# Kernel optimization log

Measured on AMD Instinct MI355X. Metric: run time of the kernel, lower is better.

## Reference

```python
import jax, jax.numpy as jnp
import numpy as np

SPU_ZERO = float(np.sqrt(0.5))  # sqrt(|spu(0)|), spu(0) = -0.5


def spu(x):
    # spu(x) = x^2 - 0.5 for x >= 0, sigmoid(-x) - 1 for x < 0
    return jnp.where(x >= 0, x * x - 0.5, jax.nn.sigmoid(-x) - 1.0)


def dspu(x):
    s = jax.nn.sigmoid(-x)
    return jnp.where(x >= 0, 2.0 * x, -s * (1.0 - s))


def setup_inputs() -> dict:
    key = jax.random.key(0)
    k1, k2, k3 = jax.random.split(key, 3)
    N = 16777216
    lower = jax.random.normal(k1, (N,), dtype=jnp.float32)
    width = jnp.abs(jax.random.normal(k2, (N,), dtype=jnp.float32)) + 1e-3
    upper = lower + width
    t = jax.random.uniform(k3, (N,), dtype=jnp.float32)
    x = lower + t * width  # concrete point inside the interval
    return {"x": x, "lower_bounds": lower, "upper_bounds": upper}


def reference(x, lower_bounds, upper_bounds):
    l = lower_bounds
    u = upper_bounds
    sl = spu(l)
    su = spu(u)
    slope = (su - sl) / (u - l)  # chord slope
    chord_b = sl - slope * l

    # case 2 (l >= 0) tangent at midpoint
    a2 = (u + l) * 0.5
    wl2 = dspu(a2)
    bl2 = spu(a2) - a2 * wl2

    # case 3 (l < 0 <= u, u >= spu_zero) tangent at max(mid, spu_zero)
    a3 = jnp.maximum(a2, SPU_ZERO)
    wl3 = dspu(a3)
    bl3 = spu(a3) - a3 * wl3

    # case 4 (l < 0, 0 < u < spu_zero)
    flat4 = sl > su
    wu4 = jnp.where(flat4, 0.0, slope)
    bu4 = jnp.where(flat4, jnp.maximum(sl, su), chord_b)

    c1 = u <= 0
    c2 = l >= 0
    c3 = u >= SPU_ZERO

    w_u = jnp.where(c1, 0.0,
          jnp.where(c2, u + l,
          jnp.where(c3, slope, wu4)))
    b_u = jnp.where(c1, sl,
          jnp.where(c2, -u * l + 0.5,  # -u*l - spu(0)
          jnp.where(c3, chord_b, bu4)))
    w_l = jnp.where(c1, slope,
          jnp.where(c2, wl2,
          jnp.where(c3, wl3, 0.0)))
    b_l = jnp.where(c1, chord_b,
          jnp.where(c2, bl2,
          jnp.where(c3, bl3, -0.5)))  # spu(0) = -0.5

    out = spu(x)
    # weights are eye with modified diagonal -> diagonal matmul is elementwise
    new_lower = w_l * l + b_l
    new_upper = w_u * u + b_u
    return (out, new_lower, new_upper)
```

## Files before the change

### kernel.cpp

```cpp
#include <hip/hip_runtime.h>
#include <math.h>

#define SPU_ZERO 0.70710678118654752440f

__device__ __forceinline__ float spu_f(float x) {
    if (x >= 0.0f) return x * x - 0.5f;
    float s = 1.0f / (1.0f + expf(x));
    return s - 1.0f;
}

__device__ __forceinline__ float dspu_f(float x) {
    if (x >= 0.0f) return 2.0f * x;
    float s = 1.0f / (1.0f + expf(x));
    return -s * (1.0f - s);
}

__device__ __forceinline__ void spu_transform(float x, float l, float u,
                                              float& o, float& nl, float& nu) {
    float sl = spu_f(l);
    float su = spu_f(u);
    float slope = (su - sl) / (u - l);
    float chord_b = sl - slope * l;

    float w_u, b_u, w_l, b_l;
    if (u <= 0.0f) {
        w_u = 0.0f;   b_u = sl;
        w_l = slope;  b_l = chord_b;
    } else if (l >= 0.0f) {
        float a2 = 0.5f * (u + l);
        float wl2 = 2.0f * a2;
        float bl2 = (a2 * a2 - 0.5f) - a2 * wl2;
        w_u = u + l;  b_u = 0.5f - u * l;
        w_l = wl2;    b_l = bl2;
    } else if (u >= SPU_ZERO) {
        float a2 = 0.5f * (u + l);
        float a3 = fmaxf(a2, SPU_ZERO);
        float wl3 = 2.0f * a3;
        float bl3 = (a3 * a3 - 0.5f) - a3 * wl3;
        w_u = slope;  b_u = chord_b;
        w_l = wl3;    b_l = bl3;
    } else {
        bool flat4 = sl > su;
        w_u = flat4 ? 0.0f : slope;
        b_u = flat4 ? fmaxf(sl, su) : chord_b;
        w_l = 0.0f;   b_l = -0.5f;
    }

    o  = spu_f(x);
    nl = w_l * l + b_l;
    nu = w_u * u + b_u;
}

__global__ void __launch_bounds__(256)
spu_kernel_v4(const float4* __restrict__ xs,
              const float4* __restrict__ ls,
              const float4* __restrict__ us,
              float4* __restrict__ out, int n4) {
    int i = blockIdx.x * blockDim.x + threadIdx.x;
    if (i >= n4) return;

    float4 xv = xs[i];
    float4 lv = ls[i];
    float4 uv = us[i];
    float4 o, nl, nu;

    spu_transform(xv.x, lv.x, uv.x, o.x, nl.x, nu.x);
    spu_transform(xv.y, lv.y, uv.y, o.y, nl.y, nu.y);
    spu_transform(xv.z, lv.z, uv.z, o.z, nl.z, nu.z);
    spu_transform(xv.w, lv.w, uv.w, o.w, nl.w, nu.w);

    out[i]           = o;
    out[n4 + i]      = nl;
    out[2 * n4 + i]  = nu;
}

__global__ void __launch_bounds__(64)
spu_kernel_tail(const float* __restrict__ xs,
                const float* __restrict__ ls,
                const float* __restrict__ us,
                float* __restrict__ out, int n, int start) {
    int i = start + blockIdx.x * blockDim.x + threadIdx.x;
    if (i >= n) return;
    float o, nl, nu;
    spu_transform(xs[i], ls[i], us[i], o, nl, nu);
    out[i]         = o;
    out[n + i]     = nl;
    out[2 * n + i] = nu;
}

extern "C" void kernel_launch(void* const* d_in, const int* in_sizes, int n_in,
                              void* d_out, int out_size, void* d_ws, size_t ws_size,
                              hipStream_t stream) {
    const float* x = (const float*)d_in[0];
    const float* l = (const float*)d_in[1];
    const float* u = (const float*)d_in[2];
    float* out = (float*)d_out;
    int n = in_sizes[0];
    int n4 = n / 4;
    int rem = n - n4 * 4;

    if (n4 > 0) {
        int blocks = (n4 + 255) / 256;
        spu_kernel_v4<<<blocks, 256, 0, stream>>>(
            (const float4*)x, (const float4*)l, (const float4*)u,
            (float4*)out, n4);
    }
    if (rem > 0) {
        spu_kernel_tail<<<1, 64, 0, stream>>>(x, l, u, out, n, n4 * 4);
    }
}
```

Before: 336.9 us.

## Use fast exp/rcp intrinsics, branchless select chain, and two float4 per thread

Replaces the IEEE expf and divisions with __expf and the hardware reciprocal, and turns the four-way case branching into a chain of predicated selects, so lanes in a wavefront no longer diverge. Each thread now loads two float4 groups up front before computing, which raises memory-level parallelism and halves the grid size. The kernel is memory-bound (about 400 MB moved), so the arithmetic changes matter less than the load batching. Fast math lowers precision slightly, and the select chain evaluates every case for every element.

```diff
diff --git a/kernel.cpp b/kernel.cpp
--- a/kernel.cpp
+++ b/kernel.cpp
@@ -3,75 +3,95 @@
 
 #define SPU_ZERO 0.70710678118654752440f
 
-__device__ __forceinline__ float spu_f(float x) {
-    if (x >= 0.0f) return x * x - 0.5f;
-    float s = 1.0f / (1.0f + expf(x));
-    return s - 1.0f;
+__device__ __forceinline__ float fast_rcp(float x) {
+    return __builtin_amdgcn_rcpf(x);
 }
 
-__device__ __forceinline__ float dspu_f(float x) {
-    if (x >= 0.0f) return 2.0f * x;
-    float s = 1.0f / (1.0f + expf(x));
-    return -s * (1.0f - s);
+__device__ __forceinline__ float spu_f(float x) {
+    float e   = __expf(x);
+    float neg = fast_rcp(1.0f + e) - 1.0f;
+    float pos = x * x - 0.5f;
+    return (x >= 0.0f) ? pos : neg;
 }
 
 __device__ __forceinline__ void spu_transform(float x, float l, float u,
                                               float& o, float& nl, float& nu) {
-    float sl = spu_f(l);
-    float su = spu_f(u);
-    float slope = (su - sl) / (u - l);
+    float sl      = spu_f(l);
+    float su      = spu_f(u);
+    float slope   = (su - sl) * fast_rcp(u - l);
     float chord_b = sl - slope * l;
 
-    float w_u, b_u, w_l, b_l;
-    if (u <= 0.0f) {
-        w_u = 0.0f;   b_u = sl;
-        w_l = slope;  b_l = chord_b;
-    } else if (l >= 0.0f) {
-        float a2 = 0.5f * (u + l);
-        float wl2 = 2.0f * a2;
-        float bl2 = (a2 * a2 - 0.5f) - a2 * wl2;
-        w_u = u + l;  b_u = 0.5f - u * l;
-        w_l = wl2;    b_l = bl2;
-    } else if (u >= SPU_ZERO) {
-        float a2 = 0.5f * (u + l);
-        float a3 = fmaxf(a2, SPU_ZERO);
-        float wl3 = 2.0f * a3;
-        float bl3 = (a3 * a3 - 0.5f) - a3 * wl3;
-        w_u = slope;  b_u = chord_b;
-        w_l = wl3;    b_l = bl3;
-    } else {
-        bool flat4 = sl > su;
-        w_u = flat4 ? 0.0f : slope;
-        b_u = flat4 ? fmaxf(sl, su) : chord_b;
-        w_l = 0.0f;   b_l = -0.5f;
-    }
+    float a2 = 0.5f * (u + l);
+    float a3 = fmaxf(a2, SPU_ZERO);
+
+    bool c1    = (u <= 0.0f);
+    bool c2    = (l >= 0.0f);
+    bool c3    = (u >= SPU_ZERO);
+    bool flat4 = (sl > su);
+
+    float w_u = flat4 ? 0.0f : slope;
+    float b_u = flat4 ? fmaxf(sl, su) : chord_b;
+    float w_l = 0.0f;
+    float b_l = -0.5f;
+
+    w_u = c3 ? slope : w_u;
+    b_u = c3 ? chord_b : b_u;
+    w_l = c3 ? 2.0f * a3 : w_l;
+    b_l = c3 ? (-(a3 * a3) - 0.5f) : b_l;
+
+    w_u = c2 ? (u + l) : w_u;
+    b_u = c2 ? (0.5f - u * l) : b_u;
+    w_l = c2 ? 2.0f * a2 : w_l;
+    b_l = c2 ? (-(a2 * a2) - 0.5f) : b_l;
+
+    w_u = c1 ? 0.0f : w_u;
+    b_u = c1 ? sl : b_u;
+    w_l = c1 ? slope : w_l;
+    b_l = c1 ? chord_b : b_l;
 
     o  = spu_f(x);
     nl = w_l * l + b_l;
     nu = w_u * u + b_u;
 }
 
-__global__ void __launch_bounds__(256)
-spu_kernel_v4(const float4* __restrict__ xs,
-              const float4* __restrict__ ls,
-              const float4* __restrict__ us,
-              float4* __restrict__ out, int n4) {
-    int i = blockIdx.x * blockDim.x + threadIdx.x;
-    if (i >= n4) return;
-
-    float4 xv = xs[i];
-    float4 lv = ls[i];
-    float4 uv = us[i];
-    float4 o, nl, nu;
-
+__device__ __forceinline__ void do_vec4(float4 xv, float4 lv, float4 uv,
+                                        float4& o, float4& nl, float4& nu) {
     spu_transform(xv.x, lv.x, uv.x, o.x, nl.x, nu.x);
     spu_transform(xv.y, lv.y, uv.y, o.y, nl.y, nu.y);
     spu_transform(xv.z, lv.z, uv.z, o.z, nl.z, nu.z);
     spu_transform(xv.w, lv.w, uv.w, o.w, nl.w, nu.w);
+}
 
-    out[i]           = o;
-    out[n4 + i]      = nl;
-    out[2 * n4 + i]  = nu;
+__global__ void __launch_bounds__(256)
+spu_kernel_v4x2(const float4* __restrict__ xs,
+                const float4* __restrict__ ls,
+                const float4* __restrict__ us,
+                float4* __restrict__ out, int n4) {
+    int stride = gridDim.x * blockDim.x;
+    int i0 = blockIdx.x * blockDim.x + threadIdx.x;
+    int i1 = i0 + stride;
+
+    bool p0 = i0 < n4;
+    bool p1 = i1 < n4;
+
+    float4 x0, l0, u0, x1, l1, u1;
+    if (p0) { x0 = xs[i0]; l0 = ls[i0]; u0 = us[i0]; }
+    if (p1) { x1 = xs[i1]; l1 = ls[i1]; u1 = us[i1]; }
+
+    if (p0) {
+        float4 o, nl, nu;
+        do_vec4(x0, l0, u0, o, nl, nu);
+        out[i0]          = o;
+        out[n4 + i0]     = nl;
+        out[2 * n4 + i0] = nu;
+    }
+    if (p1) {
+        float4 o, nl, nu;
+        do_vec4(x1, l1, u1, o, nl, nu);
+        out[i1]          = o;
+        out[n4 + i1]     = nl;
+        out[2 * n4 + i1] = nu;
+    }
 }
 
 __global__ void __launch_bounds__(64)
@@ -100,8 +120,9 @@
     int rem = n - n4 * 4;
 
     if (n4 > 0) {
-        int blocks = (n4 + 255) / 256;
-        spu_kernel_v4<<<blocks, 256, 0, stream>>>(
+        int threads_needed = (n4 + 1) / 2;
+        int blocks = (threads_needed + 255) / 256;
+        spu_kernel_v4x2<<<blocks, 256, 0, stream>>>(
             (const float4*)x, (const float4*)l, (const float4*)u,
             (float4*)out, n4);
     }
```

Result: no change. 337.2 us (+0.1%).
